# Performance work log

Measured on AMD Instinct MI355X. Metric: run time of the kernel, lower is better.

Reference implementation:

```python
import jax, jax.numpy as jnp
import numpy as np

# Config (mirrors init_kwargs)
N_PARTS = 4
N_DATASETS = 4
N_VOLUMES = 12
N_TRANSFORMS = 1
TEMP = 0.1
EPS = 1e-6
BS = N_PARTS * N_DATASETS * N_VOLUMES          # 192
N = BS * (N_TRANSFORMS + 1)                    # 384 total rows
PD = N_PARTS * N_DATASETS                      # 16
C, H, W = 32, 48, 48


def setup_inputs() -> dict:
    key = jax.random.key(0)
    k1, k2 = jax.random.split(key)
    reg_pred = jax.random.normal(k1, (N, C, H, W), dtype=jnp.float32)
    mean_representations = jax.random.normal(k2, (N_DATASETS, C, H, W), dtype=jnp.float32)
    return {"reg_pred": reg_pred, "mean_representations": mean_representations}


def reference(reg_pred, mean_representations):
    X = reg_pred.reshape(N, -1)                                  # [N, D]
    ds_id = (jnp.arange(N) // N_PARTS) % N_DATASETS              # dataset id per row
    Mn = mean_representations.reshape(N_DATASETS, -1)[ds_id]     # [N, D] per-row mean
    Z = X - Mn                                                   # demeaned
    # cosine similarity with per-vector norm clamped at eps (torch CosineSimilarity)
    nrm = jnp.maximum(jnp.linalg.norm(Z, axis=1), EPS)
    Zn = Z / nrm[:, None]
    S = (Zn @ Zn.T) / TEMP                                       # [N, N] scaled cos sims
    E = jnp.exp(S)
    # negative (denominator) set for anchor a: all j with j % PD != a % PD
    rem = jnp.arange(N) % PD
    neg_mask = rem[:, None] != rem[None, :]
    Dsum = jnp.sum(E * neg_mask, axis=1)                         # [N]

    p = jnp.arange(BS)
    i1 = p
    i2 = BS + p
    i3 = (p + PD) % N
    i4 = (BS + p + PD) % N

    def pair_loss(a, b):
        # Faithful to original: BOTH terms use the (a,b) numerator similarity
        num = S[a, b]
        en = jnp.exp(num)
        return -(num - jnp.log(en + Dsum[a])) - (num - jnp.log(en + Dsum[b]))

    total = (pair_loss(i1, i2) + pair_loss(i3, i4)
             + pair_loss(i1, i3) + pair_loss(i2, i4)).sum()
    return total / (N_TRANSFORMS * 3 * BS)
```

## Files before the change

kernel.cpp:

```cpp
#include <hip/hip_runtime.h>
#include <hip/hip_bf16.h>
#include <stdint.h>

#define NR 384
#define DD 73728
#define PDV 16
#define BSV 192
#define KSPLIT 256
#define KCH 288
#define BK 32
#define NIT 9
#define RS 40

typedef __bf16 bf16;
typedef __attribute__((ext_vector_type(4))) __bf16 bf16x4;
typedef __attribute__((ext_vector_type(8))) __bf16 bf16x8;
typedef __attribute__((ext_vector_type(4))) float f32x4;

__global__ __launch_bounds__(256, 3) void k_gram(const float* __restrict__ X,
                                                 const float* __restrict__ M,
                                                 float* __restrict__ Gp) {
    __shared__ float msh[4 * KCH];
    __shared__ bf16 ash[128 * RS];
    __shared__ bf16 bsh[128 * RS];
    const int tid  = threadIdx.x;
    const int lane = tid & 63;
    const int w    = tid >> 6;
    const int quad = lane >> 4;
    const int l15  = lane & 15;
    const int wm   = w & 1, wn = w >> 1;
    const int srow = tid >> 3;
    const int fseg = tid & 7;

    int tile = blockIdx.x % 6;
    int ks   = blockIdx.x / 6;
    int tm = (tile < 3) ? 0 : ((tile < 5) ? 1 : 2);
    int tn = (tile < 3) ? tile : ((tile < 5) ? (tile - 2) : 2);
    const bool diag = (tm == tn);
    const float* Xa = X + (size_t)(tm * 128) * DD;
    const float* Xb = X + (size_t)(tn * 128) * DD;
    const bf16* bbase = diag ? ash : bsh;
    size_t k0 = (size_t)ks * KCH;

    for (int i = tid; i < 4 * 72; i += 256) {
        int ds = i / 72;
        int c  = (i - ds * 72) * 4;
        *(float4*)&msh[ds * KCH + c] = *(const float4*)(M + (size_t)ds * DD + k0 + c);
    }

    f32x4 acc[4][4];
#pragma unroll
    for (int i = 0; i < 4; ++i)
#pragma unroll
        for (int j = 0; j < 4; ++j) acc[i][j] = (f32x4){0.f, 0.f, 0.f, 0.f};

    float4 xa[4], xb[4];
    auto load_regs = [&](int it) {
        size_t gk = k0 + (size_t)it * BK + fseg * 4;
#pragma unroll
        for (int p = 0; p < 4; ++p) {
            int row = p * 32 + srow;
            xa[p] = *(const float4*)(Xa + (size_t)row * DD + gk);
            if (!diag) xb[p] = *(const float4*)(Xb + (size_t)row * DD + gk);
        }
    };
    auto write_tiles = [&](int it) {
        int kc = it * BK + fseg * 4;
#pragma unroll
        for (int p = 0; p < 4; ++p) {
            int row = p * 32 + srow;
            float4 m4 = *(const float4*)&msh[((row >> 2) & 3) * KCH + kc];
            bf16x4 za;
            za[0] = (bf16)(xa[p].x - m4.x); za[1] = (bf16)(xa[p].y - m4.y);
            za[2] = (bf16)(xa[p].z - m4.z); za[3] = (bf16)(xa[p].w - m4.w);
            *(bf16x4*)&ash[row * RS + fseg * 4] = za;
            if (!diag) {
                bf16x4 zb;
                zb[0] = (bf16)(xb[p].x - m4.x); zb[1] = (bf16)(xb[p].y - m4.y);
                zb[2] = (bf16)(xb[p].z - m4.z); zb[3] = (bf16)(xb[p].w - m4.w);
                *(bf16x4*)&bsh[row * RS + fseg * 4] = zb;
            }
        }
    };

    load_regs(0);
    __syncthreads();
    write_tiles(0);

    for (int it = 0; it < NIT; ++it) {
        __syncthreads();
        if (it + 1 < NIT) load_regs(it + 1);
        bf16x8 af[4], bfv[4];
#pragma unroll
        for (int i = 0; i < 4; ++i) {
            int r = wm * 64 + i * 16 + l15;
            af[i] = *(const bf16x8*)&ash[r * RS + quad * 8];
        }
#pragma unroll
        for (int j = 0; j < 4; ++j) {
            int r = wn * 64 + j * 16 + l15;
            bfv[j] = *(const bf16x8*)&bbase[r * RS + quad * 8];
        }
#pragma unroll
        for (int i = 0; i < 4; ++i)
#pragma unroll
            for (int j = 0; j < 4; ++j)
                acc[i][j] = __builtin_amdgcn_mfma_f32_16x16x32_bf16(
                    af[i], bfv[j], acc[i][j], 0, 0, 0);
        __syncthreads();
        if (it + 1 < NIT) write_tiles(it + 1);
    }

    float* gp = Gp + ((size_t)(ks * 6 + tile) << 14);
#pragma unroll
    for (int i = 0; i < 4; ++i) {
        int lr0 = wm * 64 + i * 16 + quad * 4;
#pragma unroll
        for (int j = 0; j < 4; ++j) {
            int lc = wn * 64 + j * 16 + l15;
#pragma unroll
            for (int r = 0; r < 4; ++r)
                gp[(lr0 + r) * 128 + lc] = acc[i][j][r];
        }
    }
}

__global__ __launch_bounds__(256) void k_red(const float* __restrict__ Gp,
                                             float* __restrict__ G,
                                             float* __restrict__ invn,
                                             float* __restrict__ out) {
    int t    = blockIdx.x * 256 + threadIdx.x;
    if (t == 0) out[0] = 0.0f;
    int tile = t >> 14;
    int idx  = t & 16383;
    int lr   = idx >> 7, lc = idx & 127;
    const float* p = Gp + ((size_t)tile << 14) + idx;
    float s = 0.0f;
#pragma unroll 8
    for (int ks = 0; ks < KSPLIT; ++ks) s += p[(size_t)ks * 98304];
    int tm = (tile < 3) ? 0 : ((tile < 5) ? 1 : 2);
    int tn = (tile < 3) ? tile : ((tile < 5) ? (tile - 2) : 2);
    int a = tm * 128 + lr, b = tn * 128 + lc;
    G[(size_t)a * NR + b] = s;
    G[(size_t)b * NR + a] = s;
    if (a == b) invn[a] = 1.0f / fmaxf(sqrtf(s), 1e-6f);
}

__global__ __launch_bounds__(256) void k_dsum(const float* __restrict__ G,
                                              const float* __restrict__ invn,
                                              float* __restrict__ out) {
    const int lane = threadIdx.x & 63;
    const int a    = blockIdx.x * 4 + (threadIdx.x >> 6);
    float ia  = invn[a];
    int arem  = a & 15;
    float acc = 0.0f;
    for (int b = lane; b < NR; b += 64) {
        float s = G[(size_t)a * NR + b] * ia * invn[b] * 10.0f;
        if ((b & 15) != arem) acc += expf(s);
    }
#pragma unroll
    for (int o = 32; o > 0; o >>= 1) acc += __shfl_down(acc, o);
    if (lane == 0) {
        float Dsa = acc;
        int pr[4];
        if (a < 16)       { pr[0] = 192 + a; pr[1] = a + 16;  pr[2] = a + 192; pr[3] = a + 368; }
        else if (a < 192) { pr[0] = 192 + a; pr[1] = a + 16;  pr[2] = a + 192; pr[3] = a - 16; }
        else if (a < 368) { pr[0] = a - 192; pr[1] = a + 16;  pr[2] = a - 192; pr[3] = a - 16; }
        else              { pr[0] = a - 192; pr[1] = a - 368; pr[2] = a - 192; pr[3] = a - 16; }
        float t = 0.0f;
#pragma unroll
        for (int s = 0; s < 4; ++s) {
            int b = pr[s];
            float num = G[(size_t)a * NR + b] * ia * invn[b] * 10.0f;
            t += -num + logf(expf(num) + Dsa);
        }
        atomicAdd(out, t * (1.0f / 576.0f));
    }
}

extern "C" void kernel_launch(void* const* d_in, const int* in_sizes, int n_in,
                              void* d_out, int out_size, void* d_ws, size_t ws_size,
                              hipStream_t stream) {
    const float* X = (const float*)d_in[0];
    const float* M = (const float*)d_in[1];
    float* out = (float*)d_out;

    char* ws = (char*)d_ws;
    float* Gp   = (float*)ws;
    float* G    = Gp + (size_t)KSPLIT * 6 * 16384;
    float* invn = G + (size_t)NR * NR;

    k_gram<<<dim3(6 * KSPLIT), dim3(256), 0, stream>>>(X, M, Gp);
    k_red<<<dim3(384), dim3(256), 0, stream>>>(Gp, G, invn, out);
    k_dsum<<<dim3(NR / 4), dim3(256), 0, stream>>>(G, invn, out);
}
```

Measured before the change: 213.5 us.

## Use single-wave 64x64 Gram tiles with register double-buffering and XCD-aware K-split mapping

Replaces the 4-wave 128x128 upper-triangular tiling (6 tiles, K split 256) with single-wavefront 64x64 tiles (21 upper-triangular tiles, K split 96) and removes all __syncthreads. Mean vectors are loaded straight from global memory instead of being staged in LDS. Global loads are double-buffered in registers across two iterations. Block indices are mapped so that each XCD handles contiguous K-chunks. This cuts barrier overhead and the size of the partial-sum buffer, but smaller tiles reuse less data from global memory, so X traffic and register pressure both go up.

```diff
diff --git a/kernel.cpp b/kernel.cpp
--- a/kernel.cpp
+++ b/kernel.cpp
@@ -6,47 +6,45 @@
 #define DD 73728
 #define PDV 16
 #define BSV 192
-#define KSPLIT 256
-#define KCH 288
+#define KSPLIT 96
+#define KCH 768
 #define BK 32
-#define NIT 9
+#define NIT 24
 #define RS 40
+#define NTILE 21
 
 typedef __bf16 bf16;
 typedef __attribute__((ext_vector_type(4))) __bf16 bf16x4;
 typedef __attribute__((ext_vector_type(8))) __bf16 bf16x8;
 typedef __attribute__((ext_vector_type(4))) float f32x4;
 
-__global__ __launch_bounds__(256, 3) void k_gram(const float* __restrict__ X,
-                                                 const float* __restrict__ M,
-                                                 float* __restrict__ Gp) {
-    __shared__ float msh[4 * KCH];
-    __shared__ bf16 ash[128 * RS];
-    __shared__ bf16 bsh[128 * RS];
-    const int tid  = threadIdx.x;
-    const int lane = tid & 63;
-    const int w    = tid >> 6;
+__global__ __launch_bounds__(64, 2) void k_gram(const float* __restrict__ X,
+                                                const float* __restrict__ M,
+                                                float* __restrict__ Gp) {
+    __shared__ bf16 ash[64 * RS];
+    __shared__ bf16 bsh[64 * RS];
+    const int lane = threadIdx.x;
     const int quad = lane >> 4;
     const int l15  = lane & 15;
-    const int wm   = w & 1, wn = w >> 1;
-    const int srow = tid >> 3;
-    const int fseg = tid & 7;
-
-    int tile = blockIdx.x % 6;
-    int ks   = blockIdx.x / 6;
-    int tm = (tile < 3) ? 0 : ((tile < 5) ? 1 : 2);
-    int tn = (tile < 3) ? tile : ((tile < 5) ? (tile - 2) : 2);
-    const bool diag = (tm == tn);
-    const float* Xa = X + (size_t)(tm * 128) * DD;
-    const float* Xb = X + (size_t)(tn * 128) * DD;
-    const bf16* bbase = diag ? ash : bsh;
-    size_t k0 = (size_t)ks * KCH;
-
-    for (int i = tid; i < 4 * 72; i += 256) {
-        int ds = i / 72;
-        int c  = (i - ds * 72) * 4;
-        *(float4*)&msh[ds * KCH + c] = *(const float4*)(M + (size_t)ds * DD + k0 + c);
-    }
+    const int srow = lane >> 3;
+    const int fseg = lane & 7;
+    const int s2   = srow >> 2;
+
+    int xcd  = blockIdx.x & 7;
+    int g    = blockIdx.x >> 3;
+    int tile = g % NTILE;
+    int ks   = xcd + 8 * (g / NTILE);
+
+    int tp = 0, rem = tile;
+    while (rem >= 6 - tp) { rem -= 6 - tp; ++tp; }
+    int tq = tp + rem;
+    const bool diag = (tp == tq);
+
+    const float* Xa = X + (size_t)(tp * 64) * DD;
+    const float* Xb = X + (size_t)(tq * 64) * DD;
+    const float* Me = M + (size_t)s2 * DD;
+    const float* Mo = M + (size_t)(s2 + 2) * DD;
+    const size_t k0 = (size_t)ks * KCH;
 
     f32x4 acc[4][4];
 #pragma unroll
@@ -54,22 +52,28 @@
 #pragma unroll
         for (int j = 0; j < 4; ++j) acc[i][j] = (f32x4){0.f, 0.f, 0.f, 0.f};
 
-    float4 xa[4], xb[4];
-    auto load_regs = [&](int it) {
+    float4 xa0[8], xb0[8], xa1[8], xb1[8];
+    float4 me0, mo0, me1, mo1;
+
+    auto load_it = [&](int it, float4 (&xa)[8], float4 (&xb)[8],
+                       float4& me, float4& mo) {
         size_t gk = k0 + (size_t)it * BK + fseg * 4;
-#pragma unroll
-        for (int p = 0; p < 4; ++p) {
-            int row = p * 32 + srow;
-            xa[p] = *(const float4*)(Xa + (size_t)row * DD + gk);
-            if (!diag) xb[p] = *(const float4*)(Xb + (size_t)row * DD + gk);
-        }
+        me = *(const float4*)(Me + gk);
+        mo = *(const float4*)(Mo + gk);
+#pragma unroll
+        for (int p = 0; p < 8; ++p)
+            xa[p] = *(const float4*)(Xa + (size_t)(8 * p + srow) * DD + gk);
+        if (!diag)
+#pragma unroll
+            for (int p = 0; p < 8; ++p)
+                xb[p] = *(const float4*)(Xb + (size_t)(8 * p + srow) * DD + gk);
     };
-    auto write_tiles = [&](int it) {
-        int kc = it * BK + fseg * 4;
-#pragma unroll
-        for (int p = 0; p < 4; ++p) {
-            int row = p * 32 + srow;
-            float4 m4 = *(const float4*)&msh[((row >> 2) & 3) * KCH + kc];
+    auto stage_it = [&](float4 (&xa)[8], float4 (&xb)[8],
+                        float4& me, float4& mo) {
+#pragma unroll
+        for (int p = 0; p < 8; ++p) {
+            float4 m4 = (p & 1) ? mo : me;
+            int row = 8 * p + srow;
             bf16x4 za;
             za[0] = (bf16)(xa[p].x - m4.x); za[1] = (bf16)(xa[p].y - m4.y);
             za[2] = (bf16)(xa[p].z - m4.z); za[3] = (bf16)(xa[p].w - m4.w);
@@ -82,45 +86,44 @@
             }
         }
     };
-
-    load_regs(0);
-    __syncthreads();
-    write_tiles(0);
-
-    for (int it = 0; it < NIT; ++it) {
-        __syncthreads();
-        if (it + 1 < NIT) load_regs(it + 1);
+    auto compute_it = [&]() {
+        const bf16* bb = diag ? ash : bsh;
         bf16x8 af[4], bfv[4];
 #pragma unroll
-        for (int i = 0; i < 4; ++i) {
-            int r = wm * 64 + i * 16 + l15;
-            af[i] = *(const bf16x8*)&ash[r * RS + quad * 8];
-        }
-#pragma unroll
-        for (int j = 0; j < 4; ++j) {
-            int r = wn * 64 + j * 16 + l15;
-            bfv[j] = *(const bf16x8*)&bbase[r * RS + quad * 8];
-        }
+        for (int i = 0; i < 4; ++i)
+            af[i] = *(const bf16x8*)&ash[(i * 16 + l15) * RS + quad * 8];
+#pragma unroll
+        for (int j = 0; j < 4; ++j)
+            bfv[j] = *(const bf16x8*)&bb[(j * 16 + l15) * RS + quad * 8];
 #pragma unroll
         for (int i = 0; i < 4; ++i)
 #pragma unroll
             for (int j = 0; j < 4; ++j)
                 acc[i][j] = __builtin_amdgcn_mfma_f32_16x16x32_bf16(
                     af[i], bfv[j], acc[i][j], 0, 0, 0);
-        __syncthreads();
-        if (it + 1 < NIT) write_tiles(it + 1);
-    }
-
-    float* gp = Gp + ((size_t)(ks * 6 + tile) << 14);
+    };
+
+    load_it(0, xa0, xb0, me0, mo0);
+    load_it(1, xa1, xb1, me1, mo1);
+    for (int it = 0; it < NIT; it += 2) {
+        stage_it(xa0, xb0, me0, mo0);
+        if (it + 2 < NIT) load_it(it + 2, xa0, xb0, me0, mo0);
+        compute_it();
+        stage_it(xa1, xb1, me1, mo1);
+        if (it + 3 < NIT) load_it(it + 3, xa1, xb1, me1, mo1);
+        compute_it();
+    }
+
+    float* gp = Gp + (size_t)(ks * NTILE + tile) * 4096;
 #pragma unroll
     for (int i = 0; i < 4; ++i) {
-        int lr0 = wm * 64 + i * 16 + quad * 4;
+        int lr0 = i * 16 + quad * 4;
 #pragma unroll
         for (int j = 0; j < 4; ++j) {
-            int lc = wn * 64 + j * 16 + l15;
+            int lc = j * 16 + l15;
 #pragma unroll
             for (int r = 0; r < 4; ++r)
-                gp[(lr0 + r) * 128 + lc] = acc[i][j][r];
+                gp[(lr0 + r) * 64 + lc] = acc[i][j][r];
         }
     }
 }
@@ -129,18 +132,19 @@
                                              float* __restrict__ G,
                                              float* __restrict__ invn,
                                              float* __restrict__ out) {
-    int t    = blockIdx.x * 256 + threadIdx.x;
+    int t = blockIdx.x * 256 + threadIdx.x;
     if (t == 0) out[0] = 0.0f;
-    int tile = t >> 14;
-    int idx  = t & 16383;
-    int lr   = idx >> 7, lc = idx & 127;
-    const float* p = Gp + ((size_t)tile << 14) + idx;
+    int tile = t >> 12;
+    int idx  = t & 4095;
+    int lr   = idx >> 6, lc = idx & 63;
+    const float* p = Gp + (size_t)tile * 4096 + idx;
     float s = 0.0f;
 #pragma unroll 8
-    for (int ks = 0; ks < KSPLIT; ++ks) s += p[(size_t)ks * 98304];
-    int tm = (tile < 3) ? 0 : ((tile < 5) ? 1 : 2);
-    int tn = (tile < 3) ? tile : ((tile < 5) ? (tile - 2) : 2);
-    int a = tm * 128 + lr, b = tn * 128 + lc;
+    for (int ks = 0; ks < KSPLIT; ++ks) s += p[(size_t)ks * (NTILE * 4096)];
+    int tp = 0, rem = tile;
+    while (rem >= 6 - tp) { rem -= 6 - tp; ++tp; }
+    int tq = tp + rem;
+    int a = tp * 64 + lr, b = tq * 64 + lc;
     G[(size_t)a * NR + b] = s;
     G[(size_t)b * NR + a] = s;
     if (a == b) invn[a] = 1.0f / fmaxf(sqrtf(s), 1e-6f);
@@ -187,10 +191,10 @@
 
     char* ws = (char*)d_ws;
     float* Gp   = (float*)ws;
-    float* G    = Gp + (size_t)KSPLIT * 6 * 16384;
+    float* G    = Gp + (size_t)KSPLIT * NTILE * 4096;
     float* invn = G + (size_t)NR * NR;
 
-    k_gram<<<dim3(6 * KSPLIT), dim3(256), 0, stream>>>(X, M, Gp);
-    k_red<<<dim3(384), dim3(256), 0, stream>>>(Gp, G, invn, out);
+    k_gram<<<dim3(8 * NTILE * (KSPLIT / 8)), dim3(64), 0, stream>>>(X, M, Gp);
+    k_red<<<dim3(336), dim3(256), 0, stream>>>(Gp, G, invn, out);
     k_dsum<<<dim3(NR / 4), dim3(256), 0, stream>>>(G, invn, out);
 }
```

Result: faster. 209.1 us (-2.1%).
